# Performance work log

Measured on AMD Instinct MI355X. Metric: run time of the kernel, lower is better.

Reference implementation:

```python
import jax, jax.numpy as jnp
import numpy as np

B, H, S, D = 1, 16, 2048, 128
NUM_DOCS = 4


def setup_inputs() -> dict:
    key = jax.random.key(0)
    kq, kk, kv = jax.random.split(key, 3)
    q = jax.random.normal(kq, (B, H, S, D), dtype=jnp.float32)
    k = jax.random.normal(kk, (B, H, S, D), dtype=jnp.float32)
    v = jax.random.normal(kv, (B, H, S, D), dtype=jnp.float32)
    # Document boundaries within the packed sequence (as produced by _get_offsets):
    # starts at 0, ends at total token count. 4 equal docs of length 512.
    offsets = jnp.array([0, 512, 1024, 1536, 2048], dtype=jnp.int64)
    return {"q": q, "k": k, "v": v, "offsets": offsets}


def reference(q, k, v, offsets):
    # Block-causal SDPA: token i attends to token j iff j <= i and both are
    # in the same document (documents delimited by `offsets`). This matches
    # nested-tensor SDPA with is_causal=True over the jagged documents.
    _, _, S_, D_ = q.shape
    pos = jnp.arange(S_)
    seg = jnp.searchsorted(offsets, pos, side="right")  # [S] document id per token
    mask = (seg[:, None] == seg[None, :]) & (pos[None, :] <= pos[:, None])  # [S,S]
    scale = 1.0 / jnp.sqrt(jnp.asarray(D_, q.dtype))
    scores = jnp.einsum("bhsd,bhtd->bhst", q, k) * scale  # [B,H,S,S]
    scores = jnp.where(mask[None, None], scores, jnp.finfo(q.dtype).min)
    attn = jax.nn.softmax(scores, axis=-1)
    return jnp.einsum("bhst,bhtd->bhsd", attn, v)
```

## Files before the change

kernel.cpp:

```cpp
#include <hip/hip_runtime.h>
#include <hip/hip_bf16.h>
#include <math.h>

#define NH 16
#define SL 2048
#define DM 128

typedef float f32x4 __attribute__((ext_vector_type(4)));
typedef short s16x8 __attribute__((ext_vector_type(8)));
typedef short s16x4 __attribute__((ext_vector_type(4)));

static __device__ __forceinline__ short f2bf(float f) {
  __hip_bfloat16 h = __float2bfloat16(f);
  return __builtin_bit_cast(short, h);
}

__global__ __launch_bounds__(256) void attn_dbuf(
    const float* __restrict__ qg,
    const float* __restrict__ kg,
    const float* __restrict__ vg,
    const int* __restrict__ offs, int n_off,
    float* __restrict__ out)
{
  __shared__ __align__(16) char Kb[2][16384];
  __shared__ __align__(16) char Vb[2][16384];
  __shared__ __align__(16) char Pb[4][2048];

  const int t    = threadIdx.x;
  const int lane = t & 63;
  const int w    = t >> 6;
  const int col  = lane & 15;
  const int g    = lane >> 4;

  const int blk = blockIdx.x;
  const int z   = blk >> 8;
  const int y   = (blk >> 4) & 15;
  const int h   = blk & 15;
  const int dno = y >> 2, u = y & 3;
  const int p   = z ? u : 7 - u;
  const int q0  = (dno * 8 + p) * 64;

  const float* qh = qg + (size_t)h * SL * DM;
  const float* kh = kg + (size_t)h * SL * DM;
  const float* vh = vg + (size_t)h * SL * DM;

  const float scale = 0.08838834764831843f;

  const int qrow = q0 + 16 * w + col;
  int qstart = 0;
  for (int i = 0; i < n_off; ++i) { int o = offs[i]; if (o <= qrow) qstart = o; }
  int kv_lo = 0;
  for (int i = 0; i < n_off; ++i) { int o = offs[i]; if (o <= q0) kv_lo = o; }
  const int n = ((q0 + 64) - kv_lo) >> 6;

  s16x8 qf[4];
  #pragma unroll
  for (int kk = 0; kk < 4; ++kk) {
    const float* qp = qh + (size_t)qrow * DM + 32 * kk + 8 * g;
    f32x4 lo = *(const f32x4*)qp;
    f32x4 hi = *(const f32x4*)(qp + 4);
    s16x8 f;
    f[0] = f2bf(lo[0] * scale); f[1] = f2bf(lo[1] * scale);
    f[2] = f2bf(lo[2] * scale); f[3] = f2bf(lo[3] * scale);
    f[4] = f2bf(hi[0] * scale); f[5] = f2bf(hi[1] * scale);
    f[6] = f2bf(hi[2] * scale); f[7] = f2bf(hi[3] * scale);
    qf[kk] = f;
  }

  f32x4 acc[8];
  #pragma unroll
  for (int dt = 0; dt < 8; ++dt) { f32x4 zv = {0.f, 0.f, 0.f, 0.f}; acc[dt] = zv; }
  float m_ = -1e30f, l_ = 0.f;

  char* pb = &Pb[w][0];

  const int d0  = (t & 31) * 4;
  const int r0  = t >> 5;
  const int rot = (t >> 1) & 3;
  f32x4 kr[8], vr[8];

#define LOADT(T) do {                                                         \
    const float* _ks = kh + (size_t)(kv_lo + ((T) << 6)) * DM;                \
    const float* _vs = vh + (size_t)(kv_lo + ((T) << 6)) * DM;                \
    _Pragma("unroll")                                                         \
    for (int _i = 0; _i < 8; ++_i)                                            \
      kr[_i] = *(const f32x4*)(_ks + (size_t)(r0 + 8 * _i) * DM + d0);        \
    _Pragma("unroll")                                                         \
    for (int _k = 0; _k < 2; ++_k) {                                          \
      _Pragma("unroll")                                                       \
      for (int _j = 0; _j < 4; ++_j)                                          \
        vr[_k * 4 + _j] =                                                     \
          *(const f32x4*)(_vs + (size_t)(r0 * 4 + 32 * _k + _j) * DM + d0);   \
    }                                                                         \
  } while (0)

#define WRITEKV(B) do {                                                       \
    _Pragma("unroll")                                                         \
    for (int _i = 0; _i < 8; ++_i) {                                          \
      int _r = r0 + 8 * _i;                                                   \
      s16x4 _b;                                                               \
      _b[0] = f2bf(kr[_i][0]); _b[1] = f2bf(kr[_i][1]);                       \
      _b[2] = f2bf(kr[_i][2]); _b[3] = f2bf(kr[_i][3]);                       \
      *(s16x4*)(&Kb[B][0] + ((_r * 256 + d0 * 2) ^ ((_r & 7) << 4))) = _b;    \
    }                                                                         \
    _Pragma("unroll")                                                         \
    for (int _k = 0; _k < 2; ++_k) {                                          \
      int _k0 = r0 * 4 + 32 * _k;                                             \
      _Pragma("unroll")                                                       \
      for (int _di = 0; _di < 4; ++_di) {                                     \
        int _dd = (_di + rot) & 3;                                            \
        int _d  = d0 + _dd;                                                   \
        s16x4 _b;                                                             \
        _b[0] = f2bf(vr[_k * 4 + 0][_dd]); _b[1] = f2bf(vr[_k * 4 + 1][_dd]); \
        _b[2] = f2bf(vr[_k * 4 + 2][_dd]); _b[3] = f2bf(vr[_k * 4 + 3][_dd]); \
        *(s16x4*)(&Vb[B][0] + ((_d * 128 + _k0 * 2) ^ ((_d & 7) << 4))) = _b; \
      }                                                                       \
    }                                                                         \
  } while (0)

  LOADT(0);
  WRITEKV(0);
  int cur = 0;

  for (int it = 0; it < n; ++it) {
    const int kv0 = kv_lo + (it << 6);
    __syncthreads();

    const bool pre = (it + 1 < n);
    if (pre) LOADT(it + 1);
    __builtin_amdgcn_sched_barrier(0);

    f32x4 st[4];
    #pragma unroll
    for (int kt = 0; kt < 4; ++kt) { f32x4 zv = {0.f, 0.f, 0.f, 0.f}; st[kt] = zv; }
    __builtin_amdgcn_s_setprio(1);
    #pragma unroll
    for (int kt = 0; kt < 4; ++kt) {
      int row = kt * 16 + col;
      #pragma unroll
      for (int kk = 0; kk < 4; ++kk) {
        s16x8 kf = *(const s16x8*)(&Kb[cur][0] + ((row * 256 + 64 * kk + 16 * g) ^ ((row & 7) << 4)));
        st[kt] = __builtin_amdgcn_mfma_f32_16x16x32_bf16(kf, qf[kk], st[kt], 0, 0, 0);
      }
    }
    __builtin_amdgcn_s_setprio(0);

    float cm = -3.0e38f;
    #pragma unroll
    for (int kt = 0; kt < 4; ++kt) {
      #pragma unroll
      for (int r = 0; r < 4; ++r) {
        int kpos = kv0 + kt * 16 + 4 * g + r;
        float x = st[kt][r];
        bool ok = (kpos <= qrow) && (kpos >= qstart);
        x = ok ? x : -3.0e38f;
        st[kt][r] = x;
        cm = fmaxf(cm, x);
      }
    }
    cm = fmaxf(cm, __shfl_xor(cm, 16));
    cm = fmaxf(cm, __shfl_xor(cm, 32));
    float mn = fmaxf(m_, cm);
    float al = __expf(m_ - mn);
    m_ = mn;
    float psum = 0.f;
    #pragma unroll
    for (int kt = 0; kt < 4; ++kt) {
      s16x4 pk;
      #pragma unroll
      for (int r = 0; r < 4; ++r) {
        float pe = __expf(st[kt][r] - mn);
        psum += pe;
        pk[r] = f2bf(pe);
      }
      *(s16x4*)(pb + ((col * 128 + 32 * kt + 8 * g) ^ ((col & 7) << 4))) = pk;
    }
    psum += __shfl_xor(psum, 16);
    psum += __shfl_xor(psum, 32);
    l_ = l_ * al + psum;

    #pragma unroll
    for (int r = 0; r < 4; ++r) {
      float ar = __shfl(al, 4 * g + r);
      #pragma unroll
      for (int dt = 0; dt < 8; ++dt) acc[dt][r] *= ar;
    }

    asm volatile("s_waitcnt lgkmcnt(0)" ::: "memory");
    __builtin_amdgcn_sched_barrier(0);

    __builtin_amdgcn_s_setprio(1);
    #pragma unroll
    for (int ksel = 0; ksel < 2; ++ksel) {
      s16x8 pa = *(const s16x8*)(pb + ((col * 128 + 64 * ksel + 16 * g) ^ ((col & 7) << 4)));
      #pragma unroll
      for (int dt = 0; dt < 8; ++dt) {
        int d = dt * 16 + col;
        s16x8 vf = *(const s16x8*)(&Vb[cur][0] + ((d * 128 + 64 * ksel + 16 * g) ^ ((d & 7) << 4)));
        acc[dt] = __builtin_amdgcn_mfma_f32_16x16x32_bf16(pa, vf, acc[dt], 0, 0, 0);
      }
    }
    __builtin_amdgcn_s_setprio(0);

    if (pre) WRITEKV(cur ^ 1);
    cur ^= 1;
  }
#undef LOADT
#undef WRITEKV

  #pragma unroll
  for (int r = 0; r < 4; ++r) {
    float lr  = __shfl(l_, 4 * g + r);
    float inv = 1.f / lr;
    int row   = q0 + 16 * w + 4 * g + r;
    float* op = out + ((size_t)h * SL + row) * DM + col;
    #pragma unroll
    for (int dt = 0; dt < 8; ++dt) op[dt * 16] = acc[dt][r] * inv;
  }
}

extern "C" void kernel_launch(void* const* d_in, const int* in_sizes, int n_in,
                              void* d_out, int out_size, void* d_ws, size_t ws_size,
                              hipStream_t stream) {
  const float* q = (const float*)d_in[0];
  const float* k = (const float*)d_in[1];
  const float* v = (const float*)d_in[2];
  const int* offs = (const int*)d_in[3];
  const int n_off = in_sizes[3];
  float* out = (float*)d_out;

  const int blocks = NH * (SL / 64);
  attn_dbuf<<<blocks, 256, 0, stream>>>(q, k, v, offs, n_off, out);
}
```

Baseline: 29.28 us.

## Replace LDS round-trip for P fragments with cross-lane shuffles

Removes the per-wave shared-memory staging buffer for the softmax probabilities. The probabilities are now packed into bf16 pairs in registers and redistributed into the MFMA A-operand layout with __shfl. This also drops the explicit lgkmcnt wait that sat before the PV matmul. The offset search becomes a fixed 8-entry unrolled scan, which only handles up to 8 offsets. The cost is 16 shuffles per iteration, and since __shfl is implemented through ds_bpermute, LDS traffic may not actually shrink.

Result: no change. 29.84 us (+1.9%).

```diff
diff --git a/kernel.cpp b/kernel.cpp
--- a/kernel.cpp
+++ b/kernel.cpp
@@ -9,10 +9,18 @@
 typedef float f32x4 __attribute__((ext_vector_type(4)));
 typedef short s16x8 __attribute__((ext_vector_type(8)));
 typedef short s16x4 __attribute__((ext_vector_type(4)));
-
+typedef int   i32x4 __attribute__((ext_vector_type(4)));
+
+static __device__ __forceinline__ unsigned short f2bfu(float f) {
+  __hip_bfloat16 h = __float2bfloat16(f);
+  return (unsigned short)__builtin_bit_cast(short, h);
+}
 static __device__ __forceinline__ short f2bf(float f) {
   __hip_bfloat16 h = __float2bfloat16(f);
   return __builtin_bit_cast(short, h);
+}
+static __device__ __forceinline__ unsigned pack2(float lo, float hi) {
+  return (unsigned)f2bfu(lo) | ((unsigned)f2bfu(hi) << 16);
 }
 
 __global__ __launch_bounds__(256) void attn_dbuf(
@@ -24,7 +32,6 @@
 {
   __shared__ __align__(16) char Kb[2][16384];
   __shared__ __align__(16) char Vb[2][16384];
-  __shared__ __align__(16) char Pb[4][2048];
 
   const int t    = threadIdx.x;
   const int lane = t & 63;
@@ -47,10 +54,16 @@
   const float scale = 0.08838834764831843f;
 
   const int qrow = q0 + 16 * w + col;
-  int qstart = 0;
-  for (int i = 0; i < n_off; ++i) { int o = offs[i]; if (o <= qrow) qstart = o; }
-  int kv_lo = 0;
-  for (int i = 0; i < n_off; ++i) { int o = offs[i]; if (o <= q0) kv_lo = o; }
+
+  int ov[8];
+  #pragma unroll
+  for (int i = 0; i < 8; ++i) ov[i] = (i < n_off) ? offs[i] : 0x7fffffff;
+  int qstart = 0, kv_lo = 0;
+  #pragma unroll
+  for (int i = 0; i < 8; ++i) {
+    if (ov[i] <= qrow) qstart = max(qstart, ov[i]);
+    if (ov[i] <= q0)   kv_lo  = max(kv_lo, ov[i]);
+  }
   const int n = ((q0 + 64) - kv_lo) >> 6;
 
   s16x8 qf[4];
@@ -71,8 +84,6 @@
   #pragma unroll
   for (int dt = 0; dt < 8; ++dt) { f32x4 zv = {0.f, 0.f, 0.f, 0.f}; acc[dt] = zv; }
   float m_ = -1e30f, l_ = 0.f;
-
-  char* pb = &Pb[w][0];
 
   const int d0  = (t & 31) * 4;
   const int r0  = t >> 5;
@@ -122,6 +133,10 @@
   WRITEKV(0);
   int cur = 0;
 
+  const int srcA = col + 32 * (g & 1);
+  const int srcB = srcA + 16;
+  const bool hi2 = (g >> 1) != 0;
+
   for (int it = 0; it < n; ++it) {
     const int kv0 = kv_lo + (it << 6);
     __syncthreads();
@@ -164,16 +179,16 @@
     float al = __expf(m_ - mn);
     m_ = mn;
     float psum = 0.f;
+    unsigned w01[4], w23[4];
     #pragma unroll
     for (int kt = 0; kt < 4; ++kt) {
-      s16x4 pk;
-      #pragma unroll
-      for (int r = 0; r < 4; ++r) {
-        float pe = __expf(st[kt][r] - mn);
-        psum += pe;
-        pk[r] = f2bf(pe);
-      }
-      *(s16x4*)(pb + ((col * 128 + 32 * kt + 8 * g) ^ ((col & 7) << 4))) = pk;
+      float p0 = __expf(st[kt][0] - mn);
+      float p1 = __expf(st[kt][1] - mn);
+      float p2 = __expf(st[kt][2] - mn);
+      float p3 = __expf(st[kt][3] - mn);
+      psum += (p0 + p1) + (p2 + p3);
+      w01[kt] = pack2(p0, p1);
+      w23[kt] = pack2(p2, p3);
     }
     psum += __shfl_xor(psum, 16);
     psum += __shfl_xor(psum, 32);
@@ -186,13 +201,23 @@
       for (int dt = 0; dt < 8; ++dt) acc[dt][r] *= ar;
     }
 
-    asm volatile("s_waitcnt lgkmcnt(0)" ::: "memory");
-    __builtin_amdgcn_sched_barrier(0);
-
     __builtin_amdgcn_s_setprio(1);
     #pragma unroll
     for (int ksel = 0; ksel < 2; ++ksel) {
-      s16x8 pa = *(const s16x8*)(pb + ((col * 128 + 64 * ksel + 16 * g) ^ ((col & 7) << 4)));
+      unsigned a0 = __shfl(w01[2 * ksel], srcA);
+      unsigned a1 = __shfl(w01[2 * ksel + 1], srcA);
+      unsigned b0 = __shfl(w23[2 * ksel], srcA);
+      unsigned b1 = __shfl(w23[2 * ksel + 1], srcA);
+      unsigned c0 = __shfl(w01[2 * ksel], srcB);
+      unsigned c1 = __shfl(w01[2 * ksel + 1], srcB);
+      unsigned e0 = __shfl(w23[2 * ksel], srcB);
+      unsigned e1 = __shfl(w23[2 * ksel + 1], srcB);
+      i32x4 uu;
+      uu[0] = (int)(hi2 ? a1 : a0);
+      uu[1] = (int)(hi2 ? b1 : b0);
+      uu[2] = (int)(hi2 ? c1 : c0);
+      uu[3] = (int)(hi2 ? e1 : e0);
+      s16x8 pa = __builtin_bit_cast(s16x8, uu);
       #pragma unroll
       for (int dt = 0; dt < 8; ++dt) {
         int d = dt * 16 + col;
```
